# Kernel optimization log

Hardware: AMD Instinct MI355X
Metric: run time of the kernel (lower is better)

Reference implementation:

```python
import jax, jax.numpy as jnp
import numpy as np

D = 1024      # input_dim
H = 16        # head_num
HD = 64       # head_dim
HID = 4096    # mlp hidden
CUR = 512     # cur_seq
PREV = 512    # prev_seq (memory)
FULL = CUR + PREV
BS = 16
SCALE = 1.0 / (HD ** 0.5)


def setup_inputs() -> dict:
    key = jax.random.key(0)
    ks = jax.random.split(key, 20)
    def nrm(k, shape, s=0.02):
        return (jax.random.normal(k, shape) * s).astype(jnp.float32)
    inp = {
        "inputs": nrm(ks[0], (CUR, BS, D), 1.0),
        "pos_embedding": nrm(ks[1], (FULL, 1, D), 1.0),
        "u": nrm(ks[2], (H, HD)),
        "v": nrm(ks[3], (H, HD)),
        "memory": nrm(ks[4], (PREV, BS, D), 1.0),
        # causal mask: position i (query) may attend to j <= i + PREV; True = masked
        "mask": jnp.triu(jnp.ones((CUR, FULL), dtype=bool), k=PREV + 1)[:, :, None],
        # attention params (stored as (in, out); torch Linear applies x @ W.T + b)
        "Wkv": nrm(ks[5], (D, 2 * H * HD)), "bkv": jnp.zeros((2 * H * HD,), jnp.float32),
        "Wq": nrm(ks[6], (D, H * HD)), "bq": jnp.zeros((H * HD,), jnp.float32),
        "Wo": nrm(ks[7], (H * HD, D)), "bo": jnp.zeros((D,), jnp.float32),
        "Wp": nrm(ks[8], (D, H * HD)), "bp": jnp.zeros((H * HD,), jnp.float32),
        # layernorms
        "ln1_g": jnp.ones((D,), jnp.float32), "ln1_b": jnp.zeros((D,), jnp.float32),
        "ln2_g": jnp.ones((D,), jnp.float32), "ln2_b": jnp.zeros((D,), jnp.float32),
        # mlp (mlp_num=2): Linear(D,HID)+relu, Linear(HID,D)+relu
        "W1": nrm(ks[9], (D, HID)), "b1": jnp.zeros((HID,), jnp.float32),
        "W2": nrm(ks[10], (HID, D)), "b2": jnp.zeros((D,), jnp.float32),
        # GRU gates: stacked [Wr,Wz,Wg] and [Ur,Uz,Ug], no bias; bg init 2.0
        "g1_W": nrm(ks[11], (3, D, D)), "g1_U": nrm(ks[12], (3, D, D)),
        "g1_bg": jnp.full((D,), 2.0, jnp.float32),
        "g2_W": nrm(ks[13], (3, D, D)), "g2_U": nrm(ks[14], (3, D, D)),
        "g2_bg": jnp.full((D,), 2.0, jnp.float32),
    }
    return inp


def _layernorm(x, g, b, eps=1e-5):
    mu = jnp.mean(x, axis=-1, keepdims=True)
    var = jnp.mean(jnp.square(x - mu), axis=-1, keepdims=True)
    return (x - mu) * jax.lax.rsqrt(var + eps) * g + b


def _rel_shift(x):
    # x: (bs, head, cur, full) -> pad/reshape/slice trick of Transformer-XL
    b, h, c, f = x.shape
    xp = jnp.pad(x, ((0, 0), (0, 0), (0, 0), (1, 0)))      # (b,h,c,f+1)
    xp = xp.reshape(b, h, f + 1, c)
    return xp[:, :, 1:, :].reshape(b, h, c, f)


def _gru_gate(x, y, W, U, bg):
    # W, U: (3, D, D) for [r, z, g] gates; torch Linear => y @ W[i].T
    r = jax.nn.sigmoid(y @ W[0].T + x @ U[0].T)
    z = jax.nn.sigmoid(y @ W[1].T + x @ U[1].T - bg)
    h = jnp.tanh(y @ W[2].T + (r * x) @ U[2].T)
    return (1.0 - z) * x + z * h


def _attention_xl(x_cur, pos_emb, x_full, u, v, mask,
                  Wkv, bkv, Wq, bq, Wo, bo, Wp, bp):
    cur, bs, _ = x_cur.shape
    full = x_full.shape[0]
    kv = x_full @ Wkv + bkv                                  # (full, bs, 2*H*HD)
    key, value = jnp.split(kv, 2, axis=-1)
    query = x_cur @ Wq + bq                                  # (cur, bs, H*HD)
    r = (pos_emb @ Wp + bp).reshape(full, H, HD)             # (full, H, HD)

    key = key.reshape(full, bs, H, HD)
    value = value.reshape(full, bs, H, HD)
    query = query.reshape(cur, bs, H, HD)

    content = jnp.einsum('ibhd,jbhd->bhij', query + u, key)  # (bs,H,cur,full)
    position = jnp.einsum('ibhd,jhd->bhij', query + v, r)    # (bs,H,cur,full)
    position = _rel_shift(position)

    attn = (content + position) * SCALE
    # mask: (cur, full, 1) bool, True = masked
    m = mask[:, :, 0][None, None]                            # (1,1,cur,full)
    attn = jnp.where(m, -jnp.inf, attn)
    p = jax.nn.softmax(attn, axis=-1)

    out = jnp.einsum('bhij,jbhd->ibhd', p, value).reshape(cur, bs, H * HD)
    return out @ Wo + bo                                     # (cur, bs, D)


def reference(inputs, pos_embedding, u, v, memory, mask,
              Wkv, bkv, Wq, bq, Wo, bo, Wp, bp,
              ln1_g, ln1_b, ln2_g, ln2_b,
              W1, b1, W2, b2,
              g1_W, g1_U, g1_bg, g2_W, g2_U, g2_bg):
    prev = memory.shape[0]
    full_input = jnp.concatenate([memory, inputs], axis=0)   # (full, bs, D)
    x1 = _layernorm(full_input, ln1_g, ln1_b)
    a1 = _attention_xl(x1[prev:], pos_embedding, x1, u, v, mask,
                       Wkv, bkv, Wq, bq, Wo, bo, Wp, bp)
    a1 = jax.nn.relu(a1)                                     # dropout = identity (eval)
    o1 = _gru_gate(inputs, a1, g1_W, g1_U, g1_bg)
    x2 = _layernorm(o1, ln2_g, ln2_b)
    m2 = jax.nn.relu(jax.nn.relu(x2 @ W1 + b1) @ W2 + b2)    # mlp: act after every linear
    o2 = _gru_gate(o1, m2, g2_W, g2_U, g2_bg)
    return o2
```

## Files before the change

kernel.cpp:

```cpp
#include <hip/hip_runtime.h>
#include <stdint.h>

typedef _Float16 h16;
typedef __attribute__((ext_vector_type(8))) _Float16 f16x8;
typedef __attribute__((ext_vector_type(4))) _Float16 f16x4;
typedef __attribute__((ext_vector_type(4))) float f32x4;

enum { F_OBF = 1, F_BIAS = 2, F_RELU = 4, F_ACC = 8 };

#define BARRIER_MEM                                  \
  do {                                               \
    asm volatile("" ::: "memory");                   \
    __builtin_amdgcn_s_barrier();                    \
    asm volatile("" ::: "memory");                   \
  } while (0)

static __device__ __forceinline__ void gload16(const void* g, void* l) {
  __builtin_amdgcn_global_load_lds((__attribute__((address_space(1))) void*)g,
                                   (__attribute__((address_space(3))) void*)l,
                                   16, 0, 0);
}

template <int BN, int FLAGS>
__global__ __launch_bounds__(512) void gemm2_k(
    const h16* __restrict__ A, const h16* __restrict__ B,
    void* __restrict__ Cv, const float* __restrict__ bias,
    int K, int lda, int ldb, int ldc, int gm) {
  constexpr int NH = BN / 128;
  constexpr int WN = BN / 4;
  __shared__ h16 Al[2][256][64];
  __shared__ h16 Bl[2][BN][64];

  const int tid = threadIdx.x, lane = tid & 63, wid = tid >> 6;
  const int wr = wid >> 2, wn = wid & 3;
  const int ar = lane & 15, q4 = lane >> 4;

  const int nwg = gridDim.x, cpx = nwg >> 3;
  const int bid = (blockIdx.x & 7) * cpx + (blockIdx.x >> 3);
  const int mx = bid % gm, ny = bid / gm;

  const h16* Ab = A + (long)mx * 256 * lda;
  const h16* Bb = B + (long)ny * BN * ldb;

  auto stageA = [&](int buf, int half, int k0) {
#pragma unroll
    for (int l = 0; l < 2; ++l) {
      const int idx = l * 512 + tid;
      const int row = half * 128 + (idx >> 3), sl = idx & 7;
      gload16(Ab + (long)row * lda + k0 + (sl ^ (row & 7)) * 8,
              (char*)&Al[buf][0][0] + (half * 1024 + l * 512 + wid * 64) * 16);
    }
  };
  auto stageB = [&](int buf, int half, int k0) {
#pragma unroll
    for (int l = 0; l < NH; ++l) {
      const int idx = l * 512 + tid;
      const int row = half * (BN / 2) + (idx >> 3), sl = idx & 7;
      gload16(Bb + (long)row * ldb + k0 + (sl ^ (row & 7)) * 8,
              (char*)&Bl[buf][0][0] + (half * (BN * 4) + l * 512 + wid * 64) * 16);
    }
  };

  f32x4 acc[8][2 * NH] = {};
  const int nk = K >> 6;

  stageB(0, 0, 0); stageB(0, 1, 0); stageA(0, 0, 0); stageA(0, 1, 0);
  if (nk > 1) { stageB(1, 0, 64); stageB(1, 1, 64); stageA(1, 0, 64); stageA(1, 1, 64); }
  if (nk > 1) {
    if constexpr (NH == 2) asm volatile("s_waitcnt vmcnt(8)" ::: "memory");
    else                   asm volatile("s_waitcnt vmcnt(6)" ::: "memory");
  } else {
    asm volatile("s_waitcnt vmcnt(0)" ::: "memory");
  }
  BARRIER_MEM;

  for (int kt = 0; kt < nk; ++kt) {
    const int b = kt & 1;
    const int k2 = (kt + 2) << 6;
    const bool pf = (kt + 2) < nk;

    f16x8 a0[4][2], b0[NH][2];
#pragma unroll
    for (int m = 0; m < 4; ++m) {
      const int row = wr * 128 + m * 16 + ar;
#pragma unroll
      for (int ks = 0; ks < 2; ++ks)
        a0[m][ks] = *(const f16x8*)&Al[b][row][((ks * 4 + q4) ^ (row & 7)) * 8];
    }
#pragma unroll
    for (int n = 0; n < NH; ++n) {
      const int row = wn * WN + n * 16 + ar;
#pragma unroll
      for (int ks = 0; ks < 2; ++ks)
        b0[n][ks] = *(const f16x8*)&Bl[b][row][((ks * 4 + q4) ^ (row & 7)) * 8];
    }
    BARRIER_MEM;
    __builtin_amdgcn_s_setprio(1);
#pragma unroll
    for (int m = 0; m < 4; ++m)
#pragma unroll
      for (int n = 0; n < NH; ++n)
#pragma unroll
        for (int ks = 0; ks < 2; ++ks)
          acc[m][n] = __builtin_amdgcn_mfma_f32_16x16x32_f16(a0[m][ks], b0[n][ks], acc[m][n], 0, 0, 0);
    __builtin_amdgcn_s_setprio(0);
    BARRIER_MEM;

    f16x8 b1f[NH][2];
#pragma unroll
    for (int n = 0; n < NH; ++n) {
      const int row = wn * WN + (n + NH) * 16 + ar;
#pragma unroll
      for (int ks = 0; ks < 2; ++ks)
        b1f[n][ks] = *(const f16x8*)&Bl[b][row][((ks * 4 + q4) ^ (row & 7)) * 8];
    }
    BARRIER_MEM;
    __builtin_amdgcn_s_setprio(1);
#pragma unroll
    for (int m = 0; m < 4; ++m)
#pragma unroll
      for (int n = 0; n < NH; ++n)
#pragma unroll
        for (int ks = 0; ks < 2; ++ks)
          acc[m][n + NH] = __builtin_amdgcn_mfma_f32_16x16x32_f16(a0[m][ks], b1f[n][ks], acc[m][n + NH], 0, 0, 0);
    __builtin_amdgcn_s_setprio(0);
    BARRIER_MEM;

    f16x8 a1f[4][2];
#pragma unroll
    for (int m = 0; m < 4; ++m) {
      const int row = wr * 128 + (m + 4) * 16 + ar;
#pragma unroll
      for (int ks = 0; ks < 2; ++ks)
        a1f[m][ks] = *(const f16x8*)&Al[b][row][((ks * 4 + q4) ^ (row & 7)) * 8];
    }
    if (pf) { stageB(b, 0, k2); stageB(b, 1, k2); }
    BARRIER_MEM;
    __builtin_amdgcn_s_setprio(1);
#pragma unroll
    for (int m = 0; m < 4; ++m)
#pragma unroll
      for (int n = 0; n < NH; ++n)
#pragma unroll
        for (int ks = 0; ks < 2; ++ks)
          acc[m + 4][n] = __builtin_amdgcn_mfma_f32_16x16x32_f16(a1f[m][ks], b0[n][ks], acc[m + 4][n], 0, 0, 0);
    __builtin_amdgcn_s_setprio(0);
    BARRIER_MEM;

    if (pf) { stageA(b, 0, k2); stageA(b, 1, k2); }
    __builtin_amdgcn_s_setprio(1);
#pragma unroll
    for (int m = 0; m < 4; ++m)
#pragma unroll
      for (int n = 0; n < NH; ++n)
#pragma unroll
        for (int ks = 0; ks < 2; ++ks)
          acc[m + 4][n + NH] = __builtin_amdgcn_mfma_f32_16x16x32_f16(a1f[m][ks], b1f[n][ks], acc[m + 4][n + NH], 0, 0, 0);
    __builtin_amdgcn_s_setprio(0);
    if (pf) {
      if constexpr (NH == 2) asm volatile("s_waitcnt vmcnt(8)" ::: "memory");
      else                   asm volatile("s_waitcnt vmcnt(6)" ::: "memory");
    } else if (kt + 1 < nk) {
      asm volatile("s_waitcnt vmcnt(0)" ::: "memory");
    }
    BARRIER_MEM;
  }

#pragma unroll
  for (int m = 0; m < 8; ++m) {
#pragma unroll
    for (int n = 0; n < 2 * NH; ++n) {
      const int col = ny * BN + wn * WN + n * 16 + ar;
      float bv1 = 0.f;
      if (FLAGS & F_BIAS) bv1 = bias[col];
#pragma unroll
      for (int r = 0; r < 4; ++r) {
        const int row = mx * 256 + wr * 128 + m * 16 + q4 * 4 + r;
        float val = acc[m][n][r] + bv1;
        if (FLAGS & F_RELU) val = fmaxf(val, 0.f);
        if constexpr ((FLAGS & F_ACC) != 0) {
          float* p = (float*)Cv + (long)row * ldc + col;
          *p = *p + val;
        } else if constexpr ((FLAGS & F_OBF) != 0) {
          ((h16*)Cv)[(long)row * ldc + col] = (h16)val;
        } else {
          ((float*)Cv)[(long)row * ldc + col] = val;
        }
      }
    }
  }
}

__global__ __launch_bounds__(256) void fattn_k(
    const h16* __restrict__ qu, const h16* __restrict__ qv,
    const h16* __restrict__ kvb, const h16* __restrict__ vT,
    const h16* __restrict__ rb, h16* __restrict__ attn) {
  __shared__ h16 Kl[128][64];
  __shared__ h16 Psc[4][16][164];

  const int tid = threadIdx.x, lane = tid & 63, wv = tid >> 6;
  const int z = blockIdx.x, b = z >> 4, h = z & 15;
  const int i0 = blockIdx.y * 64;
  const int ar = lane & 15, q4 = lane >> 4;
  const int myrow = i0 + wv * 16;
  const h16* vTz = vT + (long)z * 64 * 1024;

  const long qoff = ((long)(myrow + ar) * 16 + b) * 1024 + h * 64 + q4 * 8;
  f16x8 quf[2], qvf[2];
  quf[0] = *(const f16x8*)&qu[qoff];
  quf[1] = *(const f16x8*)&qu[qoff + 32];
  qvf[0] = *(const f16x8*)&qv[qoff];
  qvf[1] = *(const f16x8*)&qv[qoff + 32];

  f32x4 o[4] = {};
  float mrow[4], lrow[4];
#pragma unroll
  for (int r = 0; r < 4; ++r) { mrow[r] = -3e38f; lrow[r] = 0.f; }

  const int ntiles = (i0 + 575 + 128) >> 7;

  for (int t = 0; t < ntiles; ++t) {
    const int j0 = t * 128;
    __builtin_amdgcn_s_barrier();
#pragma unroll
    for (int it = 0; it < 4; ++it) {
      const int ch = it * 256 + wv * 64 + lane;
      const int kr = ch >> 3, ks = ch & 7;
      gload16(kvb + ((long)(j0 + kr) * 16 + b) * 2048 + h * 64 + (ks ^ (kr & 7)) * 8,
              (char*)&Kl[0][0] + (it * 256 + wv * 64) * 16);
    }
    asm volatile("s_waitcnt vmcnt(0)" ::: "memory");
    __builtin_amdgcn_s_barrier();

    f32x4 acc_c[8] = {};
#pragma unroll
    for (int kd = 0; kd < 2; ++kd)
#pragma unroll
      for (int nf = 0; nf < 8; ++nf) {
        const int j = nf * 16 + ar;
        const int phys = (kd * 4 + q4) ^ (j & 7);
        const f16x8 kf = *(const f16x8*)&Kl[j][phys * 8];
        acc_c[nf] = __builtin_amdgcn_mfma_f32_16x16x32_f16(quf[kd], kf, acc_c[nf], 0, 0, 0);
      }

    const int jbase = j0 - myrow + 496;
    f32x4 acc_p[9] = {};
#pragma unroll
    for (int kd = 0; kd < 2; ++kd)
#pragma unroll
      for (int jf = 0; jf < 9; ++jf) {
        int jjr = jbase + jf * 16 + ar;
        if (jjr > 1023) jjr = 1023;
        const f16x8 rf = *(const f16x8*)&rb[(long)jjr * 1024 + h * 64 + kd * 32 + q4 * 8];
        acc_p[jf] = __builtin_amdgcn_mfma_f32_16x16x32_f16(qvf[kd], rf, acc_p[jf], 0, 0, 0);
      }
#pragma unroll
    for (int jf = 0; jf < 9; ++jf)
#pragma unroll
      for (int r = 0; r < 4; ++r)
        Psc[wv][q4 * 4 + r][jf * 16 + ar] = (h16)acc_p[jf][r];

    float p[8][4];
#pragma unroll
    for (int nf = 0; nf < 8; ++nf)
#pragma unroll
      for (int r = 0; r < 4; ++r) {
        const int iloc = q4 * 4 + r;
        const int jloc = nf * 16 + ar;
        const int band = jloc - iloc + 15;
        const float pv = (float)Psc[wv][iloc][band];
        float sv = (acc_c[nf][r] + pv) * 0.125f;
        const bool ok = (j0 + jloc) <= (myrow + iloc + 512);
        p[nf][r] = ok ? sv : -3e38f;
      }
#pragma unroll
    for (int r = 0; r < 4; ++r) {
      float tm = -3e38f;
#pragma unroll
      for (int nf = 0; nf < 8; ++nf) tm = fmaxf(tm, p[nf][r]);
      tm = fmaxf(tm, __shfl_xor(tm, 1));
      tm = fmaxf(tm, __shfl_xor(tm, 2));
      tm = fmaxf(tm, __shfl_xor(tm, 4));
      tm = fmaxf(tm, __shfl_xor(tm, 8));
      const float mn = fmaxf(mrow[r], tm);
      const float sc = __expf(mrow[r] - mn);
      mrow[r] = mn;
      float ts = 0.f;
#pragma unroll
      for (int nf = 0; nf < 8; ++nf) {
        const float e = __expf(p[nf][r] - mn);
        p[nf][r] = e;
        ts += e;
      }
      ts += __shfl_xor(ts, 1);
      ts += __shfl_xor(ts, 2);
      ts += __shfl_xor(ts, 4);
      ts += __shfl_xor(ts, 8);
      lrow[r] = lrow[r] * sc + ts;
#pragma unroll
      for (int v = 0; v < 4; ++v) o[v][r] *= sc;
    }

#pragma unroll
    for (int nf = 0; nf < 8; ++nf)
#pragma unroll
      for (int r = 0; r < 4; ++r) {
        const int iloc = q4 * 4 + r, jloc = nf * 16 + ar;
        Psc[wv][iloc][((jloc >> 3) ^ (iloc & 7)) * 8 + (jloc & 7)] = (h16)p[nf][r];
      }
#pragma unroll
    for (int ks = 0; ks < 4; ++ks) {
      const f16x8 pa = *(const f16x8*)&Psc[wv][ar][((ks * 4 + q4) ^ (ar & 7)) * 8];
#pragma unroll
      for (int vnf = 0; vnf < 4; ++vnf) {
        const int d = vnf * 16 + ar;
        const f16x8 vb = *(const f16x8*)&vTz[(long)d * 1024 + j0 + ks * 32 + q4 * 8];
        o[vnf] = __builtin_amdgcn_mfma_f32_16x16x32_f16(pa, vb, o[vnf], 0, 0, 0);
      }
    }
  }

#pragma unroll
  for (int vnf = 0; vnf < 4; ++vnf)
#pragma unroll
    for (int r = 0; r < 4; ++r) {
      const int i_ = myrow + q4 * 4 + r;
      attn[((long)i_ * 16 + b) * 1024 + h * 64 + vnf * 16 + ar] =
          (h16)(o[vnf][r] / lrow[r]);
    }
}

__global__ __launch_bounds__(256) void wtrans_k(const float* __restrict__ in,
                                                h16* __restrict__ out, int K, int N) {
  __shared__ float t[32][33];
  const int tx = threadIdx.x & 31, ty = threadIdx.x >> 5;
  const int n0 = blockIdx.x * 32, k0 = blockIdx.y * 32;
#pragma unroll
  for (int j = 0; j < 32; j += 8)
    t[ty + j][tx] = in[(long)(k0 + ty + j) * N + n0 + tx];
  __syncthreads();
#pragma unroll
  for (int j = 0; j < 32; j += 8)
    out[(long)(n0 + ty + j) * K + k0 + tx] = (h16)t[tx][ty + j];
}

__global__ __launch_bounds__(256) void cast_k(const float* __restrict__ in,
                                              h16* __restrict__ out, long n4) {
  const long i = (long)blockIdx.x * 256 + threadIdx.x;
  if (i >= n4) return;
  const float4 v = ((const float4*)in)[i];
  f16x4 o;
  o[0] = (h16)v.x; o[1] = (h16)v.y; o[2] = (h16)v.z; o[3] = (h16)v.w;
  ((f16x4*)out)[i] = o;
}

__global__ void addbias_k(const float* __restrict__ bq, const float* __restrict__ u,
                          const float* __restrict__ v, float* __restrict__ qu,
                          float* __restrict__ qv) {
  const int c = blockIdx.x * 256 + threadIdx.x;
  if (c < 1024) { qu[c] = bq[c] + u[c]; qv[c] = bq[c] + v[c]; }
}

__global__ __launch_bounds__(256) void zero_out_k(float* __restrict__ out, long n) {
  const long i = (long)blockIdx.x * 256 + threadIdx.x;
  if (i < n) out[i] = 0.f;
}

__global__ __launch_bounds__(256) void ln_k(const float* __restrict__ src0,
                                            const float* __restrict__ src1, int rows0,
                                            const float* __restrict__ g,
                                            const float* __restrict__ b,
                                            h16* __restrict__ out) {
  const int row = blockIdx.x, tid = threadIdx.x;
  const float* src = (row < rows0) ? (src0 + (long)row * 1024)
                                   : (src1 + (long)(row - rows0) * 1024);
  const float4 x = ((const float4*)src)[tid];
  float s = x.x + x.y + x.z + x.w;
  float sq = x.x * x.x + x.y * x.y + x.z * x.z + x.w * x.w;
#pragma unroll
  for (int o = 32; o > 0; o >>= 1) { s += __shfl_down(s, o); sq += __shfl_down(sq, o); }
  __shared__ float red[8];
  const int lane = tid & 63, w = tid >> 6;
  if (lane == 0) { red[w] = s; red[4 + w] = sq; }
  __syncthreads();
  s = red[0] + red[1] + red[2] + red[3];
  sq = red[4] + red[5] + red[6] + red[7];
  const float mu = s * (1.f / 1024.f);
  const float inv = rsqrtf(sq * (1.f / 1024.f) - mu * mu + 1e-5f);
  const float4 gg = ((const float4*)g)[tid], bb = ((const float4*)b)[tid];
  f16x4 o;
  o[0] = (h16)((x.x - mu) * inv * gg.x + bb.x);
  o[1] = (h16)((x.y - mu) * inv * gg.y + bb.y);
  o[2] = (h16)((x.z - mu) * inv * gg.z + bb.z);
  o[3] = (h16)((x.w - mu) * inv * gg.w + bb.w);
  ((f16x4*)(out + (long)row * 1024))[tid] = o;
}

__global__ __launch_bounds__(256) void vtrans_k(const h16* __restrict__ kv,
                                                h16* __restrict__ vT) {
  const int z = blockIdx.y, b = z >> 4, h = z & 15;
  const int j0 = blockIdx.x * 64;
  __shared__ h16 t[64][72];
  const int jj = threadIdx.x >> 3, c = threadIdx.x & 7;
#pragma unroll
  for (int half = 0; half < 2; ++half) {
    const int j = jj + half * 32;
    const f16x8 v = *(const f16x8*)(kv + ((long)(j0 + j) * 16 + b) * 2048 + 1024 + h * 64 + c * 8);
    *(f16x8*)&t[j][c * 8] = v;
  }
  __syncthreads();
#pragma unroll
  for (int half = 0; half < 2; ++half) {
    const int d = jj + half * 32;
    f16x8 o;
#pragma unroll
    for (int k = 0; k < 8; ++k) o[k] = t[c * 8 + k][d];
    *(f16x8*)(vT + ((long)z * 64 + d) * 1024 + j0 + c * 8) = o;
  }
}

__global__ __launch_bounds__(256) void gru_rx_k(const float* __restrict__ T,
                                                const float* __restrict__ x,
                                                h16* __restrict__ rx) {
  const long i = (long)blockIdx.x * 256 + threadIdx.x;
  const long row = i >> 8;
  const int c4 = (int)(i & 255);
  const float4 t = *((const float4*)(T + row * 3072) + c4);
  const float4 xx = ((const float4*)x)[i];
  f16x4 o;
  o[0] = (h16)(xx.x / (1.f + __expf(-t.x)));
  o[1] = (h16)(xx.y / (1.f + __expf(-t.y)));
  o[2] = (h16)(xx.z / (1.f + __expf(-t.z)));
  o[3] = (h16)(xx.w / (1.f + __expf(-t.w)));
  ((f16x4*)rx)[i] = o;
}

__global__ __launch_bounds__(256) void gru_out_k(const float* __restrict__ T,
                                                 const float* __restrict__ x,
                                                 const float* __restrict__ bg,
                                                 float* __restrict__ outf,
                                                 h16* __restrict__ outh) {
  const long i = (long)blockIdx.x * 256 + threadIdx.x;
  const long row = i >> 8;
  const int c4 = (int)(i & 255);
  const float4 tz = *((const float4*)(T + row * 3072 + 1024) + c4);
  const float4 th = *((const float4*)(T + row * 3072 + 2048) + c4);
  const float4 xx = ((const float4*)x)[i];
  const float4 bb = ((const float4*)bg)[c4];
  float4 o;
  {
    const float z0 = 1.f / (1.f + __expf(-(tz.x - bb.x)));
    const float z1 = 1.f / (1.f + __expf(-(tz.y - bb.y)));
    const float z2 = 1.f / (1.f + __expf(-(tz.z - bb.z)));
    const float z3 = 1.f / (1.f + __expf(-(tz.w - bb.w)));
    o.x = (1.f - z0) * xx.x + z0 * tanhf(th.x);
    o.y = (1.f - z1) * xx.y + z1 * tanhf(th.y);
    o.z = (1.f - z2) * xx.z + z2 * tanhf(th.z);
    o.w = (1.f - z3) * xx.w + z3 * tanhf(th.w);
  }
  ((float4*)outf)[i] = o;
  if (outh != nullptr) {
    f16x4 oh;
    oh[0] = (h16)o.x; oh[1] = (h16)o.y; oh[2] = (h16)o.z; oh[3] = (h16)o.w;
    ((f16x4*)outh)[i] = oh;
  }
}

extern "C" void kernel_launch(void* const* d_in, const int* in_sizes, int n_in,
                              void* d_out, int out_size, void* d_ws, size_t ws_size,
                              hipStream_t stream) {
  const float* inputs = (const float*)d_in[0];
  const float* pos    = (const float*)d_in[1];
  const float* u      = (const float*)d_in[2];
  const float* v      = (const float*)d_in[3];
  const float* memory = (const float*)d_in[4];
  const float* Wkv = (const float*)d_in[6];  const float* bkv = (const float*)d_in[7];
  const float* Wq  = (const float*)d_in[8];  const float* bq  = (const float*)d_in[9];
  const float* Wo  = (const float*)d_in[10]; const float* bo  = (const float*)d_in[11];
  const float* Wp  = (const float*)d_in[12]; const float* bp  = (const float*)d_in[13];
  const float* ln1_g = (const float*)d_in[14]; const float* ln1_b = (const float*)d_in[15];
  const float* ln2_g = (const float*)d_in[16]; const float* ln2_b = (const float*)d_in[17];
  const float* W1 = (const float*)d_in[18]; const float* b1 = (const float*)d_in[19];
  const float* W2 = (const float*)d_in[20]; const float* b2 = (const float*)d_in[21];
  const float* g1_W = (const float*)d_in[22]; const float* g1_U = (const float*)d_in[23];
  const float* g1_bg = (const float*)d_in[24];
  const float* g2_W = (const float*)d_in[25]; const float* g2_U = (const float*)d_in[26];
  const float* g2_bg = (const float*)d_in[27];
  (void)in_sizes; (void)n_in;

  const size_t MB = 1u << 20;
  const size_t NEEDED = 247 * MB;
  const dim3 blk(256);
  if (ws_size < NEEDED) {
    zero_out_k<<<(out_size + 255) / 256, blk, 0, stream>>>((float*)d_out, out_size);
    return;
  }

  char* w = (char*)d_ws;
  h16* WoT   = (h16*)(w + 0 * MB);
  h16* W1T   = (h16*)(w + 2 * MB);
  h16* W2T   = (h16*)(w + 10 * MB);
  h16* g1Wb  = (h16*)(w + 18 * MB);
  h16* g1Ub  = (h16*)(w + 24 * MB);
  h16* g2Wb  = (h16*)(w + 30 * MB);
  h16* g2Ub  = (h16*)(w + 36 * MB);
  h16* WkvT  = (h16*)(w + 42 * MB);
  h16* WqT   = (h16*)(w + 46 * MB);
  h16* WpT   = (h16*)(w + 48 * MB);
  h16* posb  = (h16*)(w + 50 * MB);
  float* bias_qu = (float*)(w + 52 * MB);
  float* bias_qv = (float*)(w + 52 * MB + 8192);
  h16* xb    = (h16*)(w + 53 * MB);
  h16* x1    = (h16*)(w + 69 * MB);
  char* Rbig =        w + 101 * MB;
  h16* qu    = (h16*)(w + 197 * MB);
  h16* qv    = (h16*)(w + 213 * MB);
  h16* rb    = (h16*)(w + 229 * MB);
  h16* attn  = (h16*)(w + 231 * MB);

  h16*   kvb  = (h16*)Rbig;
  float* Tall = (float*)Rbig;
  h16*   h1   = (h16*)Rbig;
  h16*   vT   = x1;
  h16*   a1   = qu;
  h16*   rx1  = qv;
  float* o1f  = (float*)qu;
  h16*   o1b  = attn;
  h16*   x2   = x1;
  h16*   m2   = x1 + 8L * 1024 * 1024;
  h16*   rx2  = x1;

  wtrans_k<<<dim3(64, 32), blk, 0, stream>>>(Wkv, WkvT, 1024, 2048);
  wtrans_k<<<dim3(32, 32), blk, 0, stream>>>(Wq, WqT, 1024, 1024);
  wtrans_k<<<dim3(32, 32), blk, 0, stream>>>(Wo, WoT, 1024, 1024);
  wtrans_k<<<dim3(32, 32), blk, 0, stream>>>(Wp, WpT, 1024, 1024);
  wtrans_k<<<dim3(128, 32), blk, 0, stream>>>(W1, W1T, 1024, 4096);
  wtrans_k<<<dim3(32, 128), blk, 0, stream>>>(W2, W2T, 4096, 1024);
  cast_k<<<3072, blk, 0, stream>>>(g1_W, g1Wb, 786432);
  cast_k<<<3072, blk, 0, stream>>>(g1_U, g1Ub, 786432);
  cast_k<<<3072, blk, 0, stream>>>(g2_W, g2Wb, 786432);
  cast_k<<<3072, blk, 0, stream>>>(g2_U, g2Ub, 786432);
  cast_k<<<1024, blk, 0, stream>>>(pos, posb, 262144);
  cast_k<<<8192, blk, 0, stream>>>(inputs, xb, 2097152);
  addbias_k<<<4, blk, 0, stream>>>(bq, u, v, bias_qu, bias_qv);

  ln_k<<<16384, blk, 0, stream>>>(memory, inputs, 8192, ln1_g, ln1_b, x1);

  gemm2_k<256, F_OBF | F_BIAS><<<dim3(512), dim3(512), 0, stream>>>(
      x1, WkvT, kvb, bkv, 1024, 1024, 1024, 2048, 64);
  gemm2_k<128, F_OBF | F_BIAS><<<dim3(256), dim3(512), 0, stream>>>(
      x1 + 8192L * 1024, WqT, qu, bias_qu, 1024, 1024, 1024, 1024, 32);
  gemm2_k<128, F_OBF | F_BIAS><<<dim3(256), dim3(512), 0, stream>>>(
      x1 + 8192L * 1024, WqT, qv, bias_qv, 1024, 1024, 1024, 1024, 32);
  gemm2_k<128, F_OBF | F_BIAS><<<dim3(32), dim3(512), 0, stream>>>(
      posb, WpT, rb, bp, 1024, 1024, 1024, 1024, 4);
  vtrans_k<<<dim3(16, 256), blk, 0, stream>>>(kvb, vT);

  fattn_k<<<dim3(256, 8), blk, 0, stream>>>(qu, qv, kvb, vT, rb, attn);

  gemm2_k<128, F_OBF | F_BIAS | F_RELU><<<dim3(256), dim3(512), 0, stream>>>(
      attn, WoT, a1, bo, 1024, 1024, 1024, 1024, 32);

  gemm2_k<256, 0><<<dim3(384), dim3(512), 0, stream>>>(
      a1, g1Wb, Tall, nullptr, 1024, 1024, 1024, 3072, 32);
  gemm2_k<256, F_ACC><<<dim3(256), dim3(512), 0, stream>>>(
      xb, g1Ub, Tall, nullptr, 1024, 1024, 1024, 3072, 32);
  gru_rx_k<<<8192, blk, 0, stream>>>(Tall, inputs, rx1);
  gemm2_k<128, F_ACC><<<dim3(256), dim3(512), 0, stream>>>(
      rx1, g1Ub + 2L * 1024 * 1024, Tall + 2048, nullptr, 1024, 1024, 1024, 3072, 32);
  gru_out_k<<<8192, blk, 0, stream>>>(Tall, inputs, g1_bg, o1f, o1b);

  ln_k<<<8192, blk, 0, stream>>>(o1f, o1f, 8192, ln2_g, ln2_b, x2);
  gemm2_k<256, F_OBF | F_BIAS | F_RELU><<<dim3(512), dim3(512), 0, stream>>>(
      x2, W1T, h1, b1, 1024, 1024, 1024, 4096, 32);
  gemm2_k<128, F_OBF | F_BIAS | F_RELU><<<dim3(256), dim3(512), 0, stream>>>(
      h1, W2T, m2, b2, 4096, 4096, 4096, 1024, 32);

  gemm2_k<256, 0><<<dim3(384), dim3(512), 0, stream>>>(
      m2, g2Wb, Tall, nullptr, 1024, 1024, 1024, 3072, 32);
  gemm2_k<256, F_ACC><<<dim3(256), dim3(512), 0, stream>>>(
      o1b, g2Ub, Tall, nullptr, 1024, 1024, 1024, 3072, 32);
  gru_rx_k<<<8192, blk, 0, stream>>>(Tall, o1f, rx2);
  gemm2_k<128, F_ACC><<<dim3(256), dim3(512), 0, stream>>>(
      rx2, g2Ub + 2L * 1024 * 1024, Tall + 2048, nullptr, 1024, 1024, 1024, 3072, 32);
  gru_out_k<<<8192, blk, 0, stream>>>(Tall, o1f, g2_bg, (float*)d_out, nullptr);
}
```

Baseline: 1.203 ms.

## Double-buffer K tiles and stage V in LDS in attention kernel

The attention kernel now prefetches the next K tile into a second LDS buffer while the current one is used, instead of waiting on each tile load before compute. V tiles are also loaded asynchronously into swizzled LDS, replacing direct per-lane global reads inside the PV MFMA loop. Separately, four weight-cast launches are merged into one multi-grid launch. The pipeline adds LDS use and extra barriers, which may lower occupancy.

```diff
diff --git a/kernel.cpp b/kernel.cpp
--- a/kernel.cpp
+++ b/kernel.cpp
@@ -195,7 +195,8 @@
     const h16* __restrict__ qu, const h16* __restrict__ qv,
     const h16* __restrict__ kvb, const h16* __restrict__ vT,
     const h16* __restrict__ rb, h16* __restrict__ attn) {
-  __shared__ h16 Kl[128][64];
+  __shared__ h16 Kl[2][128][64];
+  __shared__ h16 Vl[64][128];
   __shared__ h16 Psc[4][16][164];
 
   const int tid = threadIdx.x, lane = tid & 63, wv = tid >> 6;
@@ -219,18 +220,39 @@
 
   const int ntiles = (i0 + 575 + 128) >> 7;
 
-  for (int t = 0; t < ntiles; ++t) {
-    const int j0 = t * 128;
-    __builtin_amdgcn_s_barrier();
+  auto stageK = [&](int buf, int j0) {
 #pragma unroll
     for (int it = 0; it < 4; ++it) {
       const int ch = it * 256 + wv * 64 + lane;
       const int kr = ch >> 3, ks = ch & 7;
       gload16(kvb + ((long)(j0 + kr) * 16 + b) * 2048 + h * 64 + (ks ^ (kr & 7)) * 8,
-              (char*)&Kl[0][0] + (it * 256 + wv * 64) * 16);
-    }
-    asm volatile("s_waitcnt vmcnt(0)" ::: "memory");
-    __builtin_amdgcn_s_barrier();
+              (char*)&Kl[buf][0][0] + (it * 256 + wv * 64) * 16);
+    }
+  };
+  auto stageV = [&](int j0) {
+#pragma unroll
+    for (int it = 0; it < 4; ++it) {
+      const int ch = it * 256 + wv * 64 + lane;
+      const int vd = ch >> 4, vs = ch & 15;
+      gload16(vTz + (long)vd * 1024 + j0 + (vs ^ (vd & 7)) * 8,
+              (char*)&Vl[0][0] + (it * 256 + wv * 64) * 16);
+    }
+  };
+
+  stageK(0, 0);
+  asm volatile("s_waitcnt vmcnt(0)" ::: "memory");
+  __builtin_amdgcn_s_barrier();
+
+  for (int t = 0; t < ntiles; ++t) {
+    const int j0 = t * 128;
+    const int kb = t & 1;
+    const bool pk = (t + 1) < ntiles;
+
+    stageV(j0);
+    if (pk) stageK(kb ^ 1, (t + 1) * 128);
+    if (pk) asm volatile("s_waitcnt vmcnt(8)" ::: "memory");
+    else    asm volatile("s_waitcnt vmcnt(4)" ::: "memory");
+    BARRIER_MEM;
 
     f32x4 acc_c[8] = {};
 #pragma unroll
@@ -239,7 +261,7 @@
       for (int nf = 0; nf < 8; ++nf) {
         const int j = nf * 16 + ar;
         const int phys = (kd * 4 + q4) ^ (j & 7);
-        const f16x8 kf = *(const f16x8*)&Kl[j][phys * 8];
+        const f16x8 kf = *(const f16x8*)&Kl[kb][j][phys * 8];
         acc_c[nf] = __builtin_amdgcn_mfma_f32_16x16x32_f16(quf[kd], kf, acc_c[nf], 0, 0, 0);
       }
 
@@ -308,16 +330,22 @@
         const int iloc = q4 * 4 + r, jloc = nf * 16 + ar;
         Psc[wv][iloc][((jloc >> 3) ^ (iloc & 7)) * 8 + (jloc & 7)] = (h16)p[nf][r];
       }
+
+    if (pk) asm volatile("s_waitcnt vmcnt(4)" ::: "memory");
+    else    asm volatile("s_waitcnt vmcnt(0)" ::: "memory");
+    BARRIER_MEM;
+
 #pragma unroll
     for (int ks = 0; ks < 4; ++ks) {
       const f16x8 pa = *(const f16x8*)&Psc[wv][ar][((ks * 4 + q4) ^ (ar & 7)) * 8];
 #pragma unroll
       for (int vnf = 0; vnf < 4; ++vnf) {
         const int d = vnf * 16 + ar;
-        const f16x8 vb = *(const f16x8*)&vTz[(long)d * 1024 + j0 + ks * 32 + q4 * 8];
+        const f16x8 vb = *(const f16x8*)&Vl[d][((ks * 4 + q4) ^ (d & 7)) * 8];
         o[vnf] = __builtin_amdgcn_mfma_f32_16x16x32_f16(pa, vb, o[vnf], 0, 0, 0);
       }
     }
+    BARRIER_MEM;
   }
 
 #pragma unroll
@@ -348,6 +376,21 @@
                                               h16* __restrict__ out, long n4) {
   const long i = (long)blockIdx.x * 256 + threadIdx.x;
   if (i >= n4) return;
+  const float4 v = ((const float4*)in)[i];
+  f16x4 o;
+  o[0] = (h16)v.x; o[1] = (h16)v.y; o[2] = (h16)v.z; o[3] = (h16)v.w;
+  ((f16x4*)out)[i] = o;
+}
+
+__global__ __launch_bounds__(256) void cast4_k(
+    const float* __restrict__ a, const float* __restrict__ b,
+    const float* __restrict__ c, const float* __restrict__ d,
+    h16* __restrict__ oa, h16* __restrict__ ob,
+    h16* __restrict__ oc, h16* __restrict__ od, long n4) {
+  const long i = (long)blockIdx.x * 256 + threadIdx.x;
+  if (i >= n4) return;
+  const float* in = (blockIdx.y == 0) ? a : (blockIdx.y == 1) ? b : (blockIdx.y == 2) ? c : d;
+  h16* out = (blockIdx.y == 0) ? oa : (blockIdx.y == 1) ? ob : (blockIdx.y == 2) ? oc : od;
   const float4 v = ((const float4*)in)[i];
   f16x4 o;
   o[0] = (h16)v.x; o[1] = (h16)v.y; o[2] = (h16)v.z; o[3] = (h16)v.w;
@@ -536,10 +579,8 @@
   wtrans_k<<<dim3(32, 32), blk, 0, stream>>>(Wp, WpT, 1024, 1024);
   wtrans_k<<<dim3(128, 32), blk, 0, stream>>>(W1, W1T, 1024, 4096);
   wtrans_k<<<dim3(32, 128), blk, 0, stream>>>(W2, W2T, 4096, 1024);
-  cast_k<<<3072, blk, 0, stream>>>(g1_W, g1Wb, 786432);
-  cast_k<<<3072, blk, 0, stream>>>(g1_U, g1Ub, 786432);
-  cast_k<<<3072, blk, 0, stream>>>(g2_W, g2Wb, 786432);
-  cast_k<<<3072, blk, 0, stream>>>(g2_U, g2Ub, 786432);
+  cast4_k<<<dim3(3072, 4), blk, 0, stream>>>(g1_W, g1_U, g2_W, g2_U,
+                                             g1Wb, g1Ub, g2Wb, g2Ub, 786432);
   cast_k<<<1024, blk, 0, stream>>>(pos, posb, 262144);
   cast_k<<<8192, blk, 0, stream>>>(inputs, xb, 2097152);
   addbias_k<<<4, blk, 0, stream>>>(bq, u, v, bias_qu, bias_qv);
```

After: 1.118 ms. -7.1%, faster.
